# Optimization experiments

Measured on AMD Instinct MI355X. Metric: run time of the kernel, lower is better.

## Reference

```python
import math
import jax
import jax.numpy as jnp
import numpy as np

B, L, C = 16, 512, 1024
N_HEAD = 8
HEAD = C // N_HEAD


def setup_inputs() -> dict:
    key = jax.random.key(0)
    k1, k2, k3, k4, k5, k6 = jax.random.split(key, 6)
    x = jax.random.normal(k1, (B, L, C), dtype=jnp.float32)
    # binary adjacency (0/1) as float, as in graph data
    adj = jax.random.randint(k2, (B, L, L), 0, 2).astype(jnp.float32)
    W_qkv = jax.random.normal(k3, (C, 3 * C), dtype=jnp.float32) * (1.0 / math.sqrt(C))
    b_qkv = jax.random.normal(k4, (3 * C,), dtype=jnp.float32) * 0.02
    W_d = jax.random.normal(k5, (1, C), dtype=jnp.float32)
    b_d = jax.random.normal(k6, (C,), dtype=jnp.float32) * 0.02
    return {"x": x, "adj": adj, "W_qkv": W_qkv, "b_qkv": b_qkv, "W_d": W_d, "b_d": b_d}


def reference(x, adj, W_qkv, b_qkv, W_d, b_d):
    # degree gating (self.degree == True)
    degree = adj.sum(-1, keepdims=True)                      # [B,L,1]
    gate = jax.nn.sigmoid(degree @ W_d + b_d)                # [B,L,C]
    x = x * gate
    # fused qkv projection, chunk into qk / res / value
    qkv = x @ W_qkv + b_qkv                                  # [B,L,3C]
    qk, res, value = jnp.split(qkv, 3, axis=-1)
    def heads(t):                                            # [B,L,C] -> [B,H,L,hd]
        return t.reshape(B, L, N_HEAD, HEAD).transpose(0, 2, 1, 3)
    qk, res, value = heads(qk), heads(res), heads(value)
    qk = jax.nn.sigmoid(qk)
    # sigmoid-kernel attention scores
    attn = jnp.einsum("bhld,bhmd->bhlm", qk, qk) / math.sqrt(HEAD)
    # adjacency masking (rel_pos_bias == True)
    attn = jnp.where(adj[:, None, :, :] == 0, 0.0, attn)
    # sum-normalization instead of softmax
    attn = attn / (attn.sum(-1, keepdims=True) + 1e-6)
    out = jnp.einsum("bhlm,bhmd->bhld", attn, value) + res   # residual from qkv chunk
    out = out.transpose(0, 2, 1, 3).reshape(B, L, C)
    return jax.nn.relu(out)
```

## Files before the change

### kernel.cpp

```cpp
#include <hip/hip_runtime.h>
#include <math.h>

#define BDIM 16
#define LDIM 512
#define CDIM 1024
#define NH 8
#define HD 128
#define MROWS (BDIM * LDIM)
#define N3 (3 * CDIM)

typedef unsigned short u16;
typedef unsigned long long u64;
typedef short s8v __attribute__((ext_vector_type(8)));
typedef short s4v __attribute__((ext_vector_type(4)));
typedef float f32x4 __attribute__((ext_vector_type(4)));

__device__ __forceinline__ float sigmoidf_(float z) {
    return 1.0f / (1.0f + __expf(-z));
}
__device__ __forceinline__ u16 f2bf(float f) {
    union { float f; unsigned int u; } v; v.f = f;
    unsigned int u = v.u;
    unsigned int r = (u + 0x7FFFu + ((u >> 16) & 1u)) >> 16;
    return (u16)r;
}
__device__ __forceinline__ float bf2f(u16 b) {
    union { unsigned int u; float f; } v; v.u = ((unsigned int)b) << 16;
    return v.f;
}

__global__ __launch_bounds__(256) void prep_kernel(const float* __restrict__ adj,
                                                   const float* __restrict__ x,
                                                   const float* __restrict__ Wd,
                                                   const float* __restrict__ bd,
                                                   const float* __restrict__ W,
                                                   u64* __restrict__ adjbits,
                                                   u16* __restrict__ xg,
                                                   u16* __restrict__ Wt) {
    __shared__ float tile[64][65];
    int bid = blockIdx.x;
    int t = threadIdx.x;
    if (bid < MROWS) {
        int row = bid;
        int lane = t & 63, w = t >> 6;
        const float* a = adj + (size_t)row * LDIM;
        float s = 0.f;
        #pragma unroll
        for (int j = 0; j < 2; ++j) {
            int mc = j * 256 + w * 64;
            float v = a[mc + lane];
            s += v;
            u64 m = __ballot(v != 0.f);
            if (lane == 0) adjbits[(size_t)row * (LDIM / 64) + (mc >> 6)] = m;
        }
        #pragma unroll
        for (int off = 32; off > 0; off >>= 1) s += __shfl_down(s, off);
        if (lane == 0) tile[0][w] = s;
        __syncthreads();
        float d = tile[0][0] + tile[0][1] + tile[0][2] + tile[0][3];
        float4 xv = ((const float4*)(x + (size_t)row * CDIM))[t];
        float4 wv = ((const float4*)Wd)[t];
        float4 bv = ((const float4*)bd)[t];
        s4v o;
        o.x = (short)f2bf(xv.x * sigmoidf_(d * wv.x + bv.x));
        o.y = (short)f2bf(xv.y * sigmoidf_(d * wv.y + bv.y));
        o.z = (short)f2bf(xv.z * sigmoidf_(d * wv.z + bv.z));
        o.w = (short)f2bf(xv.w * sigmoidf_(d * wv.w + bv.w));
        ((s4v*)(xg + (size_t)row * CDIM))[t] = o;
    } else {
        int pb = bid - MROWS;
        int k0 = (pb & 15) * 64, n0 = (pb >> 4) * 64;
        int tx = t & 63, ty = t >> 6;
        #pragma unroll
        for (int yy = ty; yy < 64; yy += 4)
            tile[yy][tx] = W[(size_t)(k0 + yy) * N3 + n0 + tx];
        __syncthreads();
        #pragma unroll
        for (int yy = ty; yy < 64; yy += 4)
            Wt[(size_t)(n0 + yy) * CDIM + k0 + tx] = f2bf(tile[tx][yy]);
    }
}

__global__ __launch_bounds__(256, 3) void gemm_bf16_kernel(const u16* __restrict__ A,
                                                           const u16* __restrict__ Bt,
                                                           const float* __restrict__ bias,
                                                           u16* __restrict__ ksig,
                                                           u16* __restrict__ resb,
                                                           u16* __restrict__ vt) {
    __shared__ __align__(16) u16 As[128 * 64];
    __shared__ __align__(16) u16 Bs[128 * 64];
    int t = threadIdx.x;
    int m0 = blockIdx.y * 128, n0 = blockIdx.x * 128;
    int lane = t & 63, w = t >> 6;
    int i15 = lane & 15, quad = lane >> 4;
    int wm = w >> 1, wn = w & 1;

    f32x4 acc[4][4];
    #pragma unroll
    for (int i = 0; i < 4; ++i)
        #pragma unroll
        for (int j = 0; j < 4; ++j) acc[i][j] = (f32x4)(0.f);

    for (int k0 = 0; k0 < CDIM; k0 += 64) {
        #pragma unroll
        for (int p = 0; p < 4; ++p) {
            int sb = (w * 4 + p) * 64;
            int s = sb + lane;
            int row = s >> 3;
            int seg = (s & 7) ^ (row & 7);
            const u16* ga = A + (size_t)(m0 + row) * CDIM + k0 + seg * 8;
            const u16* gb = Bt + (size_t)(n0 + row) * CDIM + k0 + seg * 8;
            __builtin_amdgcn_global_load_lds(
                (const __attribute__((address_space(1))) unsigned int*)ga,
                (__attribute__((address_space(3))) unsigned int*)&As[sb * 8], 16, 0, 0);
            __builtin_amdgcn_global_load_lds(
                (const __attribute__((address_space(1))) unsigned int*)gb,
                (__attribute__((address_space(3))) unsigned int*)&Bs[sb * 8], 16, 0, 0);
        }
        __syncthreads();
        #pragma unroll
        for (int kc = 0; kc < 2; ++kc) {
            s8v aF[4], bF[4];
            #pragma unroll
            for (int mt = 0; mt < 4; ++mt) {
                int row = wm * 64 + mt * 16 + i15;
                int slot = row * 8 + ((kc * 4 + quad) ^ (i15 & 7));
                aF[mt] = *(const s8v*)&As[slot * 8];
            }
            #pragma unroll
            for (int nt = 0; nt < 4; ++nt) {
                int row = wn * 64 + nt * 16 + i15;
                int slot = row * 8 + ((kc * 4 + quad) ^ (i15 & 7));
                bF[nt] = *(const s8v*)&Bs[slot * 8];
            }
            #pragma unroll
            for (int mt = 0; mt < 4; ++mt)
                #pragma unroll
                for (int nt = 0; nt < 4; ++nt)
                    acc[mt][nt] = __builtin_amdgcn_mfma_f32_16x16x32_bf16(aF[mt], bF[nt], acc[mt][nt], 0, 0, 0);
        }
        __syncthreads();
    }

    int chunk = n0 >> 10;
    #pragma unroll
    for (int nt = 0; nt < 4; ++nt) {
        int ncol = n0 + wn * 64 + nt * 16 + i15;
        float bv = bias[ncol];
        #pragma unroll
        for (int mt = 0; mt < 4; ++mt) {
            int mbase = m0 + wm * 64 + mt * 16 + quad * 4;
            if (chunk == 0) {
                int h = (ncol >> 7) & 7, d = ncol & 127;
                #pragma unroll
                for (int r = 0; r < 4; ++r) {
                    int mrow = mbase + r;
                    int bb = mrow >> 9, l = mrow & 511;
                    ksig[(((size_t)bb * NH + h) * LDIM + l) * HD + d] = f2bf(sigmoidf_(acc[mt][nt][r] + bv));
                }
            } else if (chunk == 1) {
                #pragma unroll
                for (int r = 0; r < 4; ++r) {
                    int mrow = mbase + r;
                    resb[(size_t)mrow * CDIM + (ncol - CDIM)] = f2bf(acc[mt][nt][r] + bv);
                }
            } else {
                int h = (ncol >> 7) & 7, d = ncol & 127;
                int bb = mbase >> 9, l = mbase & 511;
                s4v pk;
                pk.x = (short)f2bf(acc[mt][nt][0] + bv);
                pk.y = (short)f2bf(acc[mt][nt][1] + bv);
                pk.z = (short)f2bf(acc[mt][nt][2] + bv);
                pk.w = (short)f2bf(acc[mt][nt][3] + bv);
                *(s4v*)&vt[(((size_t)bb * NH + h) * HD + d) * LDIM + l] = pk;
            }
        }
    }
}

__global__ __launch_bounds__(256) void attn_kernel(const u16* __restrict__ ksig,
                                                   const u16* __restrict__ vt,
                                                   const u16* __restrict__ resb,
                                                   const u64* __restrict__ adjbits,
                                                   float* __restrict__ out) {
    __shared__ __align__(16) u16 lds_ks[64 * 128];
    __shared__ __align__(16) u16 lds_vt[128 * 64];
    __shared__ __align__(16) u16 lds_ps[4][16][72];

    int t = threadIdx.x;
    int lane = t & 63, w = t >> 6;
    int i15 = lane & 15, quad = lane >> 4;
    int bid = blockIdx.x;
    int l0 = (bid >> 7) * 64;
    int b  = (bid >> 3) & 15;
    int h  = bid & 7;

    const u16* ksig_bh = ksig + ((size_t)b * NH + h) * LDIM * HD;
    const u16* vt_bh   = vt + ((size_t)b * NH + h) * HD * LDIM;
    const u64* abits   = adjbits + ((size_t)b * LDIM + l0 + w * 16 + quad * 4) * (LDIM / 64);

    s8v aQ[4];
    {
        const u16* qrow = ksig_bh + (size_t)(l0 + w * 16 + i15) * HD + quad * 8;
        #pragma unroll
        for (int kc = 0; kc < 4; ++kc) aQ[kc] = *(const s8v*)(qrow + kc * 32);
    }

    f32x4 accO[8];
    #pragma unroll
    for (int i = 0; i < 8; ++i) accO[i] = (f32x4)(0.f);
    float prs[4] = {0.f, 0.f, 0.f, 0.f};

    const float scale = 0.08838834764831845f;

    for (int m0 = 0; m0 < LDIM; m0 += 64) {
        #pragma unroll
        for (int p = 0; p < 4; ++p) {
            int sb = (w * 4 + p) * 64;
            int s = sb + lane;
            int row = s >> 4;
            int seg = (s & 15) ^ (row & 15);
            const u16* g = ksig_bh + (size_t)(m0 + row) * HD + seg * 8;
            __builtin_amdgcn_global_load_lds(
                (const __attribute__((address_space(1))) unsigned int*)g,
                (__attribute__((address_space(3))) unsigned int*)&lds_ks[sb * 8], 16, 0, 0);
        }
        #pragma unroll
        for (int p = 0; p < 4; ++p) {
            int sb = (w * 4 + p) * 64;
            int s = sb + lane;
            int row = s >> 3;
            int seg = (s & 7) ^ (row & 7);
            const u16* g = vt_bh + (size_t)row * LDIM + m0 + seg * 8;
            __builtin_amdgcn_global_load_lds(
                (const __attribute__((address_space(1))) unsigned int*)g,
                (__attribute__((address_space(3))) unsigned int*)&lds_vt[sb * 8], 16, 0, 0);
        }
        unsigned int mw0[4], mw1[4];
        #pragma unroll
        for (int r = 0; r < 4; ++r) {
            u64 wrd = abits[(size_t)r * (LDIM / 64) + (m0 >> 6)];
            mw0[r] = (unsigned int)wrd;
            mw1[r] = (unsigned int)(wrd >> 32);
        }
        __syncthreads();

        f32x4 S[4];
        #pragma unroll
        for (int nt = 0; nt < 4; ++nt) {
            S[nt] = (f32x4)(0.f);
            #pragma unroll
            for (int kc = 0; kc < 4; ++kc) {
                int row = nt * 16 + i15;
                int slot = row * 16 + ((kc * 4 + quad) ^ (row & 15));
                s8v bK = *(const s8v*)&lds_ks[slot * 8];
                S[nt] = __builtin_amdgcn_mfma_f32_16x16x32_bf16(aQ[kc], bK, S[nt], 0, 0, 0);
            }
        }

        #pragma unroll
        for (int nt = 0; nt < 4; ++nt) {
            int sh = (nt & 1) * 16 + i15;
            #pragma unroll
            for (int r = 0; r < 4; ++r) {
                unsigned int half = (nt < 2) ? mw0[r] : mw1[r];
                float p = ((half >> sh) & 1u) ? S[nt][r] * scale : 0.f;
                prs[r] += p;
                lds_ps[w][quad * 4 + r][nt * 16 + i15] = f2bf(p);
            }
        }

        {
            s8v aP[2];
            #pragma unroll
            for (int ks = 0; ks < 2; ++ks)
                aP[ks] = *(const s8v*)&lds_ps[w][i15][ks * 32 + quad * 8];
            #pragma unroll
            for (int ntd = 0; ntd < 8; ++ntd) {
                #pragma unroll
                for (int ks = 0; ks < 2; ++ks) {
                    int row = ntd * 16 + i15;
                    int slot = row * 8 + ((ks * 4 + quad) ^ (row & 7));
                    s8v bV = *(const s8v*)&lds_vt[slot * 8];
                    accO[ntd] = __builtin_amdgcn_mfma_f32_16x16x32_bf16(aP[ks], bV, accO[ntd], 0, 0, 0);
                }
            }
        }
        __syncthreads();
    }

    float inv[4];
    #pragma unroll
    for (int r = 0; r < 4; ++r) {
        float s = prs[r];
        s += __shfl_xor(s, 1);
        s += __shfl_xor(s, 2);
        s += __shfl_xor(s, 4);
        s += __shfl_xor(s, 8);
        inv[r] = 1.0f / (s + 1e-6f);
    }
    #pragma unroll
    for (int ntd = 0; ntd < 8; ++ntd) {
        int dcol = h * HD + ntd * 16 + i15;
        #pragma unroll
        for (int r = 0; r < 4; ++r) {
            size_t idx = ((size_t)b * LDIM + l0 + w * 16 + quad * 4 + r) * CDIM + dcol;
            float v = accO[ntd][r] * inv[r] + bf2f(resb[idx]);
            out[idx] = fmaxf(v, 0.f);
        }
    }
}

extern "C" void kernel_launch(void* const* d_in, const int* in_sizes, int n_in,
                              void* d_out, int out_size, void* d_ws, size_t ws_size,
                              hipStream_t stream) {
    (void)in_sizes; (void)n_in; (void)out_size; (void)ws_size;
    const float* x     = (const float*)d_in[0];
    const float* adj   = (const float*)d_in[1];
    const float* W_qkv = (const float*)d_in[2];
    const float* b_qkv = (const float*)d_in[3];
    const float* W_d   = (const float*)d_in[4];
    const float* b_d   = (const float*)d_in[5];
    float* out = (float*)d_out;

    char* ws = (char*)d_ws;
    size_t off = 0;
    u64* adjb   = (u64*)(ws + off);   off += (size_t)MROWS * 8 * 8;
    u16*   xg   = (u16*)(ws + off);   off += (size_t)MROWS * CDIM * 2;
    u16*   Wt   = (u16*)(ws + off);   off += (size_t)N3 * CDIM * 2;
    u16*   ksig = (u16*)(ws + off);   off += (size_t)MROWS * CDIM * 2;
    u16*   resb = (u16*)(ws + off);   off += (size_t)MROWS * CDIM * 2;
    u16*   vt   = (u16*)(ws + off);   off += (size_t)MROWS * CDIM * 2;

    prep_kernel<<<MROWS + (CDIM / 64) * (N3 / 64), 256, 0, stream>>>(
        adj, x, W_d, b_d, W_qkv, adjb, xg, Wt);
    gemm_bf16_kernel<<<dim3(N3 / 128, MROWS / 128), 256, 0, stream>>>(xg, Wt, b_qkv, ksig, resb, vt);
    attn_kernel<<<LDIM / 64 * NH * BDIM, 256, 0, stream>>>(ksig, vt, resb, adjb, out);
}
```

Measured before the change: 208.3 us.

## Double-buffer K and V tiles in LDS to prefetch the next chunk during compute

The attention kernel gets two LDS buffers each for the K and V tiles, and its key loop is fully unrolled by hand. After each barrier it issues async global-to-LDS loads for the next 64-key chunk into the idle buffer, then runs the score and PV MFMAs on the current buffer. This removes one barrier per iteration and is meant to hide global load latency behind compute. In exchange LDS use per block roughly doubles, which can lower occupancy. The compiler may also add conservative waitcnts on the LDS DMA that cancel the overlap.

```diff
diff --git a/kernel.cpp b/kernel.cpp
--- a/kernel.cpp
+++ b/kernel.cpp
@@ -183,8 +183,10 @@
                                                    const u16* __restrict__ resb,
                                                    const u64* __restrict__ adjbits,
                                                    float* __restrict__ out) {
-    __shared__ __align__(16) u16 lds_ks[64 * 128];
-    __shared__ __align__(16) u16 lds_vt[128 * 64];
+    __shared__ __align__(16) u16 ks0[64 * 128];
+    __shared__ __align__(16) u16 ks1[64 * 128];
+    __shared__ __align__(16) u16 vt0[128 * 64];
+    __shared__ __align__(16) u16 vt1[128 * 64];
     __shared__ __align__(16) u16 lds_ps[4][16][72];
 
     int t = threadIdx.x;
@@ -213,81 +215,101 @@
 
     const float scale = 0.08838834764831845f;
 
-    for (int m0 = 0; m0 < LDIM; m0 += 64) {
-        #pragma unroll
-        for (int p = 0; p < 4; ++p) {
-            int sb = (w * 4 + p) * 64;
-            int s = sb + lane;
-            int row = s >> 4;
-            int seg = (s & 15) ^ (row & 15);
-            const u16* g = ksig_bh + (size_t)(m0 + row) * HD + seg * 8;
-            __builtin_amdgcn_global_load_lds(
-                (const __attribute__((address_space(1))) unsigned int*)g,
-                (__attribute__((address_space(3))) unsigned int*)&lds_ks[sb * 8], 16, 0, 0);
-        }
-        #pragma unroll
-        for (int p = 0; p < 4; ++p) {
-            int sb = (w * 4 + p) * 64;
-            int s = sb + lane;
-            int row = s >> 3;
-            int seg = (s & 7) ^ (row & 7);
-            const u16* g = vt_bh + (size_t)row * LDIM + m0 + seg * 8;
-            __builtin_amdgcn_global_load_lds(
-                (const __attribute__((address_space(1))) unsigned int*)g,
-                (__attribute__((address_space(3))) unsigned int*)&lds_vt[sb * 8], 16, 0, 0);
-        }
-        unsigned int mw0[4], mw1[4];
-        #pragma unroll
-        for (int r = 0; r < 4; ++r) {
-            u64 wrd = abits[(size_t)r * (LDIM / 64) + (m0 >> 6)];
-            mw0[r] = (unsigned int)wrd;
-            mw1[r] = (unsigned int)(wrd >> 32);
-        }
-        __syncthreads();
-
-        f32x4 S[4];
-        #pragma unroll
-        for (int nt = 0; nt < 4; ++nt) {
-            S[nt] = (f32x4)(0.f);
-            #pragma unroll
-            for (int kc = 0; kc < 4; ++kc) {
-                int row = nt * 16 + i15;
-                int slot = row * 16 + ((kc * 4 + quad) ^ (row & 15));
-                s8v bK = *(const s8v*)&lds_ks[slot * 8];
-                S[nt] = __builtin_amdgcn_mfma_f32_16x16x32_bf16(aQ[kc], bK, S[nt], 0, 0, 0);
-            }
-        }
-
-        #pragma unroll
-        for (int nt = 0; nt < 4; ++nt) {
-            int sh = (nt & 1) * 16 + i15;
-            #pragma unroll
-            for (int r = 0; r < 4; ++r) {
-                unsigned int half = (nt < 2) ? mw0[r] : mw1[r];
-                float p = ((half >> sh) & 1u) ? S[nt][r] * scale : 0.f;
-                prs[r] += p;
-                lds_ps[w][quad * 4 + r][nt * 16 + i15] = f2bf(p);
-            }
-        }
-
-        {
-            s8v aP[2];
-            #pragma unroll
-            for (int ks = 0; ks < 2; ++ks)
-                aP[ks] = *(const s8v*)&lds_ps[w][i15][ks * 32 + quad * 8];
-            #pragma unroll
-            for (int ntd = 0; ntd < 8; ++ntd) {
-                #pragma unroll
-                for (int ks = 0; ks < 2; ++ks) {
-                    int row = ntd * 16 + i15;
-                    int slot = row * 8 + ((ks * 4 + quad) ^ (row & 7));
-                    s8v bV = *(const s8v*)&lds_vt[slot * 8];
-                    accO[ntd] = __builtin_amdgcn_mfma_f32_16x16x32_bf16(aP[ks], bV, accO[ntd], 0, 0, 0);
-                }
-            }
-        }
-        __syncthreads();
-    }
+    int stk_row = (w * 4 * 64) >> 4;
+
+#define STAGE_K(KS, MM)                                                              \
+    {                                                                                \
+        _Pragma("unroll")                                                            \
+        for (int p = 0; p < 4; ++p) {                                                \
+            int sb = (w * 4 + p) * 64;                                               \
+            int s_ = sb + lane;                                                      \
+            int row_ = s_ >> 4;                                                      \
+            int seg_ = (s_ & 15) ^ (row_ & 15);                                      \
+            const u16* g_ = ksig_bh + (size_t)((MM) + row_) * HD + seg_ * 8;         \
+            __builtin_amdgcn_global_load_lds(                                        \
+                (const __attribute__((address_space(1))) unsigned int*)g_,           \
+                (__attribute__((address_space(3))) unsigned int*)&KS[sb * 8], 16, 0, 0); \
+        }                                                                            \
+    }
+#define STAGE_V(VT, MM)                                                              \
+    {                                                                                \
+        _Pragma("unroll")                                                            \
+        for (int p = 0; p < 4; ++p) {                                                \
+            int sb = (w * 4 + p) * 64;                                               \
+            int s_ = sb + lane;                                                      \
+            int row_ = s_ >> 3;                                                      \
+            int seg_ = (s_ & 7) ^ (row_ & 7);                                        \
+            const u16* g_ = vt_bh + (size_t)row_ * LDIM + (MM) + seg_ * 8;           \
+            __builtin_amdgcn_global_load_lds(                                        \
+                (const __attribute__((address_space(1))) unsigned int*)g_,           \
+                (__attribute__((address_space(3))) unsigned int*)&VT[sb * 8], 16, 0, 0); \
+        }                                                                            \
+    }
+#define DO_CHUNK(KS, VT, MM, STAGE_NEXT)                                             \
+    {                                                                                \
+        unsigned int mw0[4], mw1[4];                                                 \
+        _Pragma("unroll")                                                            \
+        for (int r = 0; r < 4; ++r) {                                                \
+            u64 wrd = abits[(size_t)r * (LDIM / 64) + ((MM) >> 6)];                  \
+            mw0[r] = (unsigned int)wrd;                                              \
+            mw1[r] = (unsigned int)(wrd >> 32);                                      \
+        }                                                                            \
+        __syncthreads();      \
+        STAGE_NEXT;           \
+        f32x4 S[4];                                                                  \
+        _Pragma("unroll")                                                            \
+        for (int nt = 0; nt < 4; ++nt) {                                             \
+            S[nt] = (f32x4)(0.f);                                                    \
+            _Pragma("unroll")                                                        \
+            for (int kc = 0; kc < 4; ++kc) {                                         \
+                int row_ = nt * 16 + i15;                                            \
+                int slot_ = row_ * 16 + ((kc * 4 + quad) ^ (row_ & 15));             \
+                s8v bK = *(const s8v*)&KS[slot_ * 8];                                \
+                S[nt] = __builtin_amdgcn_mfma_f32_16x16x32_bf16(aQ[kc], bK, S[nt], 0, 0, 0); \
+            }                                                                        \
+        }                                                                            \
+        _Pragma("unroll")                                                            \
+        for (int nt = 0; nt < 4; ++nt) {                                             \
+            int sh_ = (nt & 1) * 16 + i15;                                           \
+            _Pragma("unroll")                                                        \
+            for (int r = 0; r < 4; ++r) {                                            \
+                unsigned int half_ = (nt < 2) ? mw0[r] : mw1[r];                     \
+                float p_ = ((half_ >> sh_) & 1u) ? S[nt][r] * scale : 0.f;           \
+                prs[r] += p_;                                                        \
+                lds_ps[w][quad * 4 + r][nt * 16 + i15] = f2bf(p_);                   \
+            }                                                                        \
+        }                                                                            \
+        {                                                                            \
+            s8v aP[2];                                                               \
+            _Pragma("unroll")                                                        \
+            for (int ks = 0; ks < 2; ++ks)                                           \
+                aP[ks] = *(const s8v*)&lds_ps[w][i15][ks * 32 + quad * 8];           \
+            _Pragma("unroll")                                                        \
+            for (int ntd = 0; ntd < 8; ++ntd) {                                      \
+                _Pragma("unroll")                                                    \
+                for (int ks = 0; ks < 2; ++ks) {                                     \
+                    int row_ = ntd * 16 + i15;                                       \
+                    int slot_ = row_ * 8 + ((ks * 4 + quad) ^ (row_ & 7));           \
+                    s8v bV = *(const s8v*)&VT[slot_ * 8];                            \
+                    accO[ntd] = __builtin_amdgcn_mfma_f32_16x16x32_bf16(aP[ks], bV, accO[ntd], 0, 0, 0); \
+                }                                                                    \
+            }                                                                        \
+        }                                                                            \
+    }
+
+    (void)stk_row;
+    STAGE_K(ks0, 0) STAGE_V(vt0, 0)
+    DO_CHUNK(ks0, vt0, 0,   STAGE_K(ks1, 64)  STAGE_V(vt1, 64))
+    DO_CHUNK(ks1, vt1, 64,  STAGE_K(ks0, 128) STAGE_V(vt0, 128))
+    DO_CHUNK(ks0, vt0, 128, STAGE_K(ks1, 192) STAGE_V(vt1, 192))
+    DO_CHUNK(ks1, vt1, 192, STAGE_K(ks0, 256) STAGE_V(vt0, 256))
+    DO_CHUNK(ks0, vt0, 256, STAGE_K(ks1, 320) STAGE_V(vt1, 320))
+    DO_CHUNK(ks1, vt1, 320, STAGE_K(ks0, 384) STAGE_V(vt0, 384))
+    DO_CHUNK(ks0, vt0, 384, STAGE_K(ks1, 448) STAGE_V(vt1, 448))
+    DO_CHUNK(ks1, vt1, 448, )
+#undef STAGE_K
+#undef STAGE_V
+#undef DO_CHUNK
 
     float inv[4];
     #pragma unroll
```

After: 225.2 us. 1.08x slower.
